# Kernel tuning notes

Hardware: AMD Instinct MI355X
Metric: run time of the kernel (lower is better)

The kernel has to match this reference:

```python
import jax, jax.numpy as jnp
import numpy as np

DT = 600.0          # integration time step (s)
STEPS = 20          # number of Euler steps
R_EARTH = 6371000.0
DEG2RAD = np.pi / 180.0
KERNEL = jnp.array([[1.0, 2.0, 1.0], [2.0, 4.0, 2.0], [1.0, 2.0, 1.0]], dtype=jnp.float32) / 16.0


def setup_inputs() -> dict:
    key = jax.random.key(0)
    kT, ku, kv, km = jax.random.split(key, 4)
    B, H, W = 8, 360, 720  # 0.5-degree global grid
    T = jax.random.normal(kT, (B, H, W), dtype=jnp.float32)
    ug = jax.random.normal(ku, (B, H, W), dtype=jnp.float32) * 0.5
    vg = jax.random.normal(kv, (B, H, W), dtype=jnp.float32) * 0.5
    lat = (90.0 - 0.25 - jnp.arange(H, dtype=jnp.float32) * 0.5)
    lon = jnp.arange(W, dtype=jnp.float32) * 0.5
    mask = (jax.random.uniform(km, (H, W)) > 0.3).astype(jnp.float32)  # ocean mask
    return {"T": T, "ug": ug, "vg": vg, "lat": lat, "lon": lon, "mask": mask}


def _horizontal_filter(field, mask):
    # field: (B, H, W); 3x3 binomial smoothing, zero ('valid'-style) padding=1, then mask
    k = KERNEL.reshape(1, 1, 3, 3).astype(field.dtype)
    f = jax.lax.conv_general_dilated(field[:, None, :, :], k, window_strides=(1, 1),
                                     padding=((1, 1), (1, 1)))
    return f[:, 0] * mask


def reference(T, ug, vg, lat, lon, mask):
    B, H, W = T.shape
    dlat = lat[1] - lat[0]
    dlon = lon[1] - lon[0]
    dy = R_EARTH * DEG2RAD * jnp.abs(dlat)
    sign_y = jnp.where(dlat > 0, 1.0, -1.0).astype(T.dtype)
    # dx varies with latitude: (H, 1) broadcasts over (B, H, W)
    dx = (R_EARTH * DEG2RAD * dlon) * jnp.cos(lat * DEG2RAD)[:, None]
    maskb = mask[None, :, :]

    def step(Tc, _):
        # boundary-aware meridional derivative
        top = (Tc[:, 1:2, :] - Tc[:, 0:1, :]) / dy
        bot = (Tc[:, -1:, :] - Tc[:, -2:-1, :]) / dy
        mid = (Tc[:, 2:, :] - Tc[:, :-2, :]) / (2.0 * dy)
        dT_dy = jnp.concatenate([top, mid, bot], axis=1) * sign_y
        # periodic zonal derivative
        dT_dx = (jnp.roll(Tc, -1, axis=2) - jnp.roll(Tc, 1, axis=2)) / (2.0 * dx)
        advection = ug * dT_dx + vg * dT_dy
        Tn = Tc - DT * advection * maskb  # Euler update with F = -advection*mask
        Tn = _horizontal_filter(Tn, maskb)
        return Tn, None

    T_final, _ = jax.lax.scan(step, T, None, length=STEPS)
    return T_final
```

## Files before the change

kernel.cpp:

```cpp
#include <hip/hip_runtime.h>

#define H 360
#define W 720
#define NB 8
#define XC 3
#define YC 10
#define TX 240
#define TY 36
#define BPB (XC*YC)
#define WR 52
#define LST 260
#define DTS 600.0f
#define REARTH 6371000.0f
#define D2R 0.017453292519943295f

#define NQ1 (WR*64)
#define NHALO 1168
#define NGROUPS 5
#define FLAG_STRIDE 32

static __device__ __forceinline__ float2 ldc8(const float* p) {
    unsigned long long u = __hip_atomic_load((const unsigned long long*)p,
                                             __ATOMIC_RELAXED, __HIP_MEMORY_SCOPE_AGENT);
    return __builtin_bit_cast(float2, u);
}
static __device__ __forceinline__ void stc8(float* p, float2 v) {
    __hip_atomic_store((unsigned long long*)p, __builtin_bit_cast(unsigned long long, v),
                       __ATOMIC_RELAXED, __HIP_MEMORY_SCOPE_AGENT);
}

__global__ __launch_bounds__(512, 2) void ocean_persist(
    const float* __restrict__ Tin, const float* __restrict__ ug,
    const float* __restrict__ vg, const float* __restrict__ lat,
    const float* __restrict__ lon, const float* __restrict__ mask,
    float* __restrict__ out, float* __restrict__ wsf, int* __restrict__ flags)
{
    __shared__ float sT[WR * LST];

    const int tid = threadIdx.x;
    const int b  = blockIdx.z;
    const int bx = blockIdx.x * TX;
    const int by = blockIdx.y * TY;
    const int plane = H * W;

    const float dlat = lat[1] - lat[0];
    const float dy   = REARTH * D2R * fabsf(dlat);
    const float sgn  = (dlat > 0.f) ? 1.f : -1.f;
    const float dlon = lon[1] - lon[0];
    const float i2dy = 0.5f / dy, i1dy = 1.f / dy;

    const float* Tb = Tin + b * plane;
    const float* ub = ug  + b * plane;
    const float* vb = vg  + b * plane;
    float* outb = out + b * plane;
    float* wsb  = wsf + b * plane;

    int* bflags = flags + b * BPB * FLAG_STRIDE;
    int* myflag = bflags + (blockIdx.y * XC + blockIdx.x) * FLAG_STRIDE;

    const int cq = tid & 63;
    const int rg = tid >> 6;
    const int c0 = cq << 2;
    const int a  = 1 + 6 * rg;
    const int gj0 = (bx - 8 + c0 + W) % W;
    const bool hlzb = (gj0 == 0);
    const bool hrzb = (gj0 + 3 == W - 1);
    const bool topB = (blockIdx.y == 0), botB = (blockIdx.y == YC - 1);

    int goff1[7], lds1o[7];
    #pragma unroll
    for (int k = 0; k < 7; ++k) {
        const int q = tid + 512 * k;
        if (q < NQ1) {
            const int r = q >> 6, cc0 = (q & 63) << 2;
            int gi = by - 8 + r; gi = min(max(gi, 0), H - 1);
            const int gj = (bx - 8 + cc0 + W) % W;
            goff1[k] = gi * W + gj;
            lds1o[k] = r * LST + cc0;
        } else goff1[k] = -1;
    }

    int hgo[3], hlo[3];
    #pragma unroll
    for (int t = 0; t < 3; ++t) {
        const int q = tid + 512 * t;
        if (q < NHALO) {
            int r, cc0;
            if (q < 1024) { const int ri = q >> 6; r = (ri < 8) ? ri : 36 + ri; cc0 = (q & 63) << 2; }
            else { const int u = q - 1024; r = 8 + (u >> 2); const int qi = u & 3;
                   cc0 = (qi < 2) ? (qi << 2) : (248 + ((qi - 2) << 2)); }
            int gi = by - 8 + r; gi = min(max(gi, 0), H - 1);
            const int gj = (bx - 8 + cc0 + W) % W;
            hgo[t] = gi * W + gj;
            hlo[t] = r * LST + cc0;
        } else hgo[t] = -1;
    }

    float cuA[8][4], cvA[8][4];
    unsigned domm = 0;
    #pragma unroll
    for (int j = 0; j < 8; ++j) {
        #pragma unroll
        for (int t = 0; t < 4; ++t) { cuA[j][t] = 0.f; cvA[j][t] = 0.f; }
        const int gi = by - 8 + a + j;
        if ((unsigned)gi < H) {
            const float dxv  = REARTH * D2R * dlon * cosf(lat[gi] * D2R);
            const float rdx2 = 0.5f / dxv;
            const float ivy  = (gi == 0 || gi == H - 1) ? i1dy : i2dy;
            #pragma unroll
            for (int t = 0; t < 4; ++t) {
                const int off = gi * W + gj0 + t;
                const float mk = mask[off];
                cuA[j][t] = -DTS * mk * ub[off] * rdx2;
                cvA[j][t] = -DTS * mk * vb[off] * sgn * ivy;
            }
            domm |= 1u << j;
        }
    }

    float m16A[6][4];
    int o3A[6];
    unsigned outm = 0, tilem = 0, ringm = 0;
    #pragma unroll
    for (int i = 0; i < 6; ++i) {
        const int n = 2 + 6 * rg + i;
        const int gi = by - 8 + n;
        o3A[i] = 0;
        #pragma unroll
        for (int t = 0; t < 4; ++t)
            m16A[i][t] = ((unsigned)gi < H) ? mask[gi * W + gj0 + t] * (1.f / 16.f) : 0.f;
        if ((unsigned)gi < H) outm |= 1u << i;
        const bool inTile = (n >= 8 && n <= 43 && cq >= 2 && cq <= 61);
        if (inTile) {
            o3A[i] = gi * W + bx + c0 - 8;
            tilem |= 1u << i;
            if (n <= 15 || n >= 36 || cq <= 3 || cq >= 60) ringm |= 1u << i;
        }
    }

    const int* nbrF = myflag;
    if (tid < 8) {
        int dyn, dxn;
        if (tid < 3)      { dyn = -1; dxn = tid - 1; }
        else if (tid == 3){ dyn = 0;  dxn = -1; }
        else if (tid == 4){ dyn = 0;  dxn = 1; }
        else              { dyn = 1;  dxn = tid - 6; }
        const int ny = (int)blockIdx.y + dyn;
        const int nx = ((int)blockIdx.x + dxn + XC) % XC;
        if (ny >= 0 && ny < YC) nbrF = bflags + (ny * XC + nx) * FLAG_STRIDE;
    }

    #pragma unroll
    for (int k = 0; k < 7; ++k)
        if (goff1[k] >= 0)
            *(float4*)(sT + lds1o[k]) = *(const float4*)(Tb + goff1[k]);
    __syncthreads();

    auto substep = [&](bool finalOut, float* ring) {
        float4 hA[8];
        float4 m1 = *(const float4*)(sT + (a - 1) * LST + c0);
        float4 cc = *(const float4*)(sT + a * LST + c0);
        #pragma unroll
        for (int j = 0; j < 8; ++j) {
            const float4 vD = *(const float4*)(sT + (a + j + 1) * LST + c0);
            const float tl = __shfl_up(cc.w, 1);
            const float tr = __shfl_down(cc.x, 1);
            const bool dj = (domm >> j) & 1;
            float4 o;
            o.x = (dj ? cc.x : 0.f) + cuA[j][0]*(cc.y - tl)   + cvA[j][0]*(vD.x - m1.x);
            o.y = (dj ? cc.y : 0.f) + cuA[j][1]*(cc.z - cc.x) + cvA[j][1]*(vD.y - m1.y);
            o.z = (dj ? cc.z : 0.f) + cuA[j][2]*(cc.w - cc.y) + cvA[j][2]*(vD.z - m1.z);
            o.w = (dj ? cc.w : 0.f) + cuA[j][3]*(tr   - cc.z) + cvA[j][3]*(vD.w - m1.w);
            float hl = __shfl_up(o.w, 1);
            float hr = __shfl_down(o.x, 1);
            if (hlzb) hl = 0.f;
            if (hrzb) hr = 0.f;
            hA[j].x = hl  + 2.f * o.x + o.y;
            hA[j].y = o.x + 2.f * o.y + o.z;
            hA[j].z = o.y + 2.f * o.z + o.w;
            hA[j].w = o.z + 2.f * o.w + hr;
            m1 = cc; cc = vD;
        }
        __syncthreads();
        #pragma unroll
        for (int i = 0; i < 6; ++i) {
            const float4 hm = hA[i], hc = hA[i + 1], hp = hA[i + 2];
            float4 o;
            o.x = (hm.x + 2.f * hc.x + hp.x) * m16A[i][0];
            o.y = (hm.y + 2.f * hc.y + hp.y) * m16A[i][1];
            o.z = (hm.z + 2.f * hc.z + hp.z) * m16A[i][2];
            o.w = (hm.w + 2.f * hc.w + hp.w) * m16A[i][3];
            if (!finalOut) {
                if ((outm >> i) & 1)
                    *(float4*)(sT + (2 + 6 * rg + i) * LST + c0) = o;
                if (topB && rg == 1 && i == 0) *(float4*)(sT + 7  * LST + c0) = o;
                if (botB && rg == 6 && i == 5) *(float4*)(sT + 44 * LST + c0) = o;
            } else if ((tilem >> i) & 1) {
                *(float4*)(outb + o3A[i]) = o;
            }
            if (ring && ((ringm >> i) & 1)) {
                float2 lo; lo.x = o.x; lo.y = o.y;
                float2 hi; hi.x = o.z; hi.y = o.w;
                stc8(ring + o3A[i], lo);
                stc8(ring + o3A[i] + 2, hi);
            }
        }
        __syncthreads();
    };

    #pragma unroll 1
    for (int g = 0; g < NGROUPS; ++g) {
        if (g) {
            __syncthreads();
            if (tid == 0)
                __hip_atomic_store(myflag, g, __ATOMIC_RELAXED, __HIP_MEMORY_SCOPE_AGENT);
            if (tid < 64) {
                long long t0 = (long long)clock64();
                for (;;) {
                    const int v = (tid < 8)
                        ? __hip_atomic_load(nbrF, __ATOMIC_RELAXED, __HIP_MEMORY_SCOPE_AGENT)
                        : 0x7fffffff;
                    if (__all(v >= g)) break;
                    __builtin_amdgcn_s_sleep(1);
                    if ((long long)clock64() - t0 > 200000000LL) break;
                }
            }
            __syncthreads();
            const float* prev = ((g - 1) & 1) ? wsb : outb;
            #pragma unroll
            for (int t = 0; t < 3; ++t) {
                if (hgo[t] >= 0) {
                    const float2 lo = ldc8(prev + hgo[t]);
                    const float2 hi = ldc8(prev + hgo[t] + 2);
                    float4 v; v.x = lo.x; v.y = lo.y; v.z = hi.x; v.w = hi.y;
                    *(float4*)(sT + hlo[t]) = v;
                }
            }
            __syncthreads();
        }
        const bool lastG = (g == NGROUPS - 1);
        float* ring = lastG ? nullptr : ((g & 1) ? wsb : outb);
        substep(false, nullptr);
        substep(false, nullptr);
        substep(false, nullptr);
        substep(lastG, ring);
    }
}

extern "C" void kernel_launch(void* const* d_in, const int* in_sizes, int n_in,
                              void* d_out, int out_size, void* d_ws, size_t ws_size,
                              hipStream_t stream)
{
    const float* T    = (const float*)d_in[0];
    const float* ug   = (const float*)d_in[1];
    const float* vg   = (const float*)d_in[2];
    const float* lat  = (const float*)d_in[3];
    const float* lon  = (const float*)d_in[4];
    const float* mask = (const float*)d_in[5];
    float* out = (float*)d_out;

    int*   flags = (int*)d_ws;
    float* wsf   = (float*)((char*)d_ws + 65536);

    hipMemsetAsync(d_ws, 0, 65536, stream);

    ocean_persist<<<dim3(XC, YC, NB), dim3(512), 0, stream>>>(
        T, ug, vg, lat, lon, mask, out, wsf, flags);
}
```

Baseline: 141.0 us.

## Double-buffer LDS tile across substeps and use DPP lane shifts

```diff
diff --git a/kernel.cpp b/kernel.cpp
--- a/kernel.cpp
+++ b/kernel.cpp
@@ -10,6 +10,7 @@
 #define BPB (XC*YC)
 #define WR 52
 #define LST 260
+#define LSZ (WR*LST)
 #define DTS 600.0f
 #define REARTH 6371000.0f
 #define D2R 0.017453292519943295f
@@ -27,6 +28,15 @@
 static __device__ __forceinline__ void stc8(float* p, float2 v) {
     __hip_atomic_store((unsigned long long*)p, __builtin_bit_cast(unsigned long long, v),
                        __ATOMIC_RELAXED, __HIP_MEMORY_SCOPE_AGENT);
+}
+
+static __device__ __forceinline__ float dpp_up1(float x) {
+    return __builtin_bit_cast(float, __builtin_amdgcn_update_dpp(
+        0, __builtin_bit_cast(int, x), 0x138 , 0xF, 0xF, true));
+}
+static __device__ __forceinline__ float dpp_dn1(float x) {
+    return __builtin_bit_cast(float, __builtin_amdgcn_update_dpp(
+        0, __builtin_bit_cast(int, x), 0x130 , 0xF, 0xF, true));
 }
 
 __global__ __launch_bounds__(512, 2) void ocean_persist(
@@ -35,7 +45,7 @@
     const float* __restrict__ lon, const float* __restrict__ mask,
     float* __restrict__ out, float* __restrict__ wsf, int* __restrict__ flags)
 {
-    __shared__ float sT[WR * LST];
+    __shared__ float sT[2 * LSZ];
 
     const int tid = threadIdx.x;
     const int b  = blockIdx.z;
@@ -152,27 +162,32 @@
 
     #pragma unroll
     for (int k = 0; k < 7; ++k)
-        if (goff1[k] >= 0)
-            *(float4*)(sT + lds1o[k]) = *(const float4*)(Tb + goff1[k]);
+        if (goff1[k] >= 0) {
+            const float4 v = *(const float4*)(Tb + goff1[k]);
+            *(float4*)(sT + lds1o[k])       = v;
+            *(float4*)(sT + LSZ + lds1o[k]) = v;
+        }
     __syncthreads();
 
-    auto substep = [&](bool finalOut, float* ring) {
+    auto substep = [&](int p, bool finalOut, float* ring) {
+        const float* cur = sT + p * LSZ;
+        float* nxt = sT + (p ^ 1) * LSZ;
         float4 hA[8];
-        float4 m1 = *(const float4*)(sT + (a - 1) * LST + c0);
-        float4 cc = *(const float4*)(sT + a * LST + c0);
+        float4 m1 = *(const float4*)(cur + (a - 1) * LST + c0);
+        float4 cc = *(const float4*)(cur + a * LST + c0);
         #pragma unroll
         for (int j = 0; j < 8; ++j) {
-            const float4 vD = *(const float4*)(sT + (a + j + 1) * LST + c0);
-            const float tl = __shfl_up(cc.w, 1);
-            const float tr = __shfl_down(cc.x, 1);
+            const float4 vD = *(const float4*)(cur + (a + j + 1) * LST + c0);
+            const float tl = dpp_up1(cc.w);
+            const float tr = dpp_dn1(cc.x);
             const bool dj = (domm >> j) & 1;
             float4 o;
             o.x = (dj ? cc.x : 0.f) + cuA[j][0]*(cc.y - tl)   + cvA[j][0]*(vD.x - m1.x);
             o.y = (dj ? cc.y : 0.f) + cuA[j][1]*(cc.z - cc.x) + cvA[j][1]*(vD.y - m1.y);
             o.z = (dj ? cc.z : 0.f) + cuA[j][2]*(cc.w - cc.y) + cvA[j][2]*(vD.z - m1.z);
             o.w = (dj ? cc.w : 0.f) + cuA[j][3]*(tr   - cc.z) + cvA[j][3]*(vD.w - m1.w);
-            float hl = __shfl_up(o.w, 1);
-            float hr = __shfl_down(o.x, 1);
+            float hl = dpp_up1(o.w);
+            float hr = dpp_dn1(o.x);
             if (hlzb) hl = 0.f;
             if (hrzb) hr = 0.f;
             hA[j].x = hl  + 2.f * o.x + o.y;
@@ -181,7 +196,6 @@
             hA[j].w = o.z + 2.f * o.w + hr;
             m1 = cc; cc = vD;
         }
-        __syncthreads();
         #pragma unroll
         for (int i = 0; i < 6; ++i) {
             const float4 hm = hA[i], hc = hA[i + 1], hp = hA[i + 2];
@@ -192,9 +206,9 @@
             o.w = (hm.w + 2.f * hc.w + hp.w) * m16A[i][3];
             if (!finalOut) {
                 if ((outm >> i) & 1)
-                    *(float4*)(sT + (2 + 6 * rg + i) * LST + c0) = o;
-                if (topB && rg == 1 && i == 0) *(float4*)(sT + 7  * LST + c0) = o;
-                if (botB && rg == 6 && i == 5) *(float4*)(sT + 44 * LST + c0) = o;
+                    *(float4*)(nxt + (2 + 6 * rg + i) * LST + c0) = o;
+                if (topB && rg == 1 && i == 0) *(float4*)(nxt + 7  * LST + c0) = o;
+                if (botB && rg == 6 && i == 5) *(float4*)(nxt + 44 * LST + c0) = o;
             } else if ((tilem >> i) & 1) {
                 *(float4*)(outb + o3A[i]) = o;
             }
@@ -240,10 +254,10 @@
         }
         const bool lastG = (g == NGROUPS - 1);
         float* ring = lastG ? nullptr : ((g & 1) ? wsb : outb);
-        substep(false, nullptr);
-        substep(false, nullptr);
-        substep(false, nullptr);
-        substep(lastG, ring);
+        substep(0, false, nullptr);
+        substep(1, false, nullptr);
+        substep(0, false, nullptr);
+        substep(1, lastG, ring);
     }
 }
 
```

Result: faster. 137.2 us (-2.7%).
